# Optimization experiments

Measured on AMD Instinct MI355X. Metric: run time of the kernel, lower is better.

The kernel has to match this reference:

```python
import jax, jax.numpy as jnp
import numpy as np

B, C, H, W = 4, 256, 64, 64
HID = C // 2


def setup_inputs() -> dict:
    key = jax.random.key(0)
    kx, kp, kt, kg, km = jax.random.split(key, 5)
    return {
        "x": jax.random.normal(kx, (B, C, H, W), dtype=jnp.float32),
        "w_phi": jax.random.normal(kp, (HID, C), dtype=jnp.float32) * 0.02,
        "w_theta": jax.random.normal(kt, (HID, C), dtype=jnp.float32) * 0.02,
        "w_g": jax.random.normal(kg, (HID, C), dtype=jnp.float32) * 0.02,
        "w_mask": jax.random.normal(km, (C, HID), dtype=jnp.float32) * 0.02,
    }


def reference(x, w_phi, w_theta, w_g, w_mask):
    b, c, h, w = x.shape
    n = h * w
    xf = x.reshape(b, c, n)                     # [B,C,N]
    # 1x1 convs == channel GEMMs
    phi = jnp.einsum('oc,bcn->bon', w_phi, xf)      # [B,HID,N]
    theta = jnp.einsum('oc,bcn->bon', w_theta, xf)  # [B,HID,N]
    g = jnp.einsum('oc,bcn->bon', w_g, xf)          # [B,HID,N]
    # attn[b,n,m] = sum_c theta[b,c,n] * phi[b,c,m]   (theta^T @ phi)
    attn = jnp.einsum('bcn,bcm->bnm', theta, phi)   # [B,N,N]
    # Faithful to nn.Softmax(dim=1): normalize over axis 1 (theta index)
    attn = jax.nn.softmax(attn, axis=1)
    # attn_g[b,n,c] = sum_m attn[b,n,m] * g[b,c,m]   (attn @ g^T)
    attn_g = jnp.einsum('bnm,bcm->bcn', attn, g)    # [B,HID,N] (already transposed back)
    mask = jnp.einsum('oc,bcn->bon', w_mask, attn_g).reshape(b, c, h, w)
    return mask + x
```

## Files before the change

kernel.cpp:

```cpp
#include <hip/hip_runtime.h>


#define NB   4
#define CIN  256
#define HIDN 128
#define NPIX 4096

typedef __attribute__((ext_vector_type(8))) short short8;
typedef __attribute__((ext_vector_type(4))) float f32x4;
typedef __attribute__((ext_vector_type(16))) float f32x16;

__device__ __forceinline__ unsigned short f2bf(float f) {
    unsigned u = __builtin_bit_cast(unsigned, f);
    u += 0x7fffu + ((u >> 16) & 1u);
    return (unsigned short)(u >> 16);
}
__device__ __forceinline__ unsigned f2bf2(float lo, float hi) {
    return (unsigned)f2bf(lo) | ((unsigned)f2bf(hi) << 16);
}
__device__ __forceinline__ float bf2f(unsigned short s) {
    return __builtin_bit_cast(float, (unsigned)s << 16);
}
__device__ __forceinline__ void cp16(void* lds, const void* g) {
    __builtin_amdgcn_global_load_lds(
        (const __attribute__((address_space(1))) unsigned int*)g,
        (__attribute__((address_space(3))) unsigned int*)lds, 16, 0, 0);
}

__global__ __launch_bounds__(256) void k_prep_w(
    const float* __restrict__ wp, const float* __restrict__ wt,
    const float* __restrict__ wg, const float* __restrict__ wm,
    unsigned short* __restrict__ Wp, unsigned short* __restrict__ Wt,
    unsigned short* __restrict__ Wg, unsigned short* __restrict__ Wm)
{
    const int which = blockIdx.x >> 3;
    const float* src = (which == 0) ? wp : (which == 1) ? wt : (which == 2) ? wg : wm;
    unsigned short* dst = (which == 0) ? Wp : (which == 1) ? Wt : (which == 2) ? Wg : Wm;
#pragma unroll
    for (int t = 0; t < 2; ++t) {
        const int gidx = ((blockIdx.x & 7) * 256 + threadIdx.x) * 2 + t;
        int o, srcc, dstc;
        if (which < 3) {
            o = gidx >> 5;
            const int gc = gidx & 31;
            const int sg = (gc & ~15) | ((gc & 15) ^ (o & 15));
            srcc = o * 256 + gc * 8; dstc = o * 256 + sg * 8;
        } else {
            o = gidx >> 4;
            const int gc = gidx & 15;
            const int sg = gc ^ (o & 15);
            srcc = o * 128 + gc * 8; dstc = o * 128 + sg * 8;
        }
        float4 a = *(const float4*)&src[srcc];
        float4 b = *(const float4*)&src[srcc + 4];
        uint4 v;
        v.x = f2bf2(a.x, a.y); v.y = f2bf2(a.z, a.w);
        v.z = f2bf2(b.x, b.y); v.w = f2bf2(b.z, b.w);
        *(uint4*)&dst[dstc] = v;
    }
}

__global__ __launch_bounds__(256) void k_prep_x(
    const float* __restrict__ x,
    unsigned short* __restrict__ xT,
    float* __restrict__ colsum)
{
    const int nt = blockIdx.x, ct = blockIdx.y, b = blockIdx.z;
    const int tid = threadIdx.x;
    if (ct == 0 && tid < 64) colsum[(size_t)b * NPIX + nt * 64 + tid] = 0.f;

    __shared__ unsigned short Ls[64][66];
    {
        const int c_loc = tid >> 2, n_seg = (tid & 3) * 16;
        const float* src = x + ((size_t)(b * CIN + ct * 64 + c_loc)) * NPIX + nt * 64 + n_seg;
#pragma unroll
        for (int j = 0; j < 8; ++j)
            *(unsigned*)&Ls[c_loc][n_seg + 2 * j] = f2bf2(src[2 * j], src[2 * j + 1]);
    }
    __syncthreads();
    {
        const int n_loc = tid >> 2, c_seg = (tid & 3) * 16;
        const int n_glob = nt * 64 + n_loc;
        unsigned short tmp[16];
#pragma unroll
        for (int j = 0; j < 16; ++j) tmp[j] = Ls[c_seg + j][n_loc];
#pragma unroll
        for (int gr = 0; gr < 2; ++gr) {
            const int c_base = ct * 64 + c_seg + gr * 8;
            const int sec = c_base >> 7;
            const int sg = (((c_base >> 3) & 15) ^ (n_glob & 15));
            *(uint4*)&xT[((size_t)b * NPIX + n_glob) * CIN + sec * 128 + sg * 8] =
                *(uint4*)&tmp[gr * 8];
        }
    }
}

__global__ __launch_bounds__(256, 3) void k_proj(
    const unsigned short* __restrict__ Wp,
    const unsigned short* __restrict__ Wt,
    const unsigned short* __restrict__ Wg,
    const unsigned short* __restrict__ xT,
    unsigned short* __restrict__ phiT,
    unsigned short* __restrict__ thetaT,
    unsigned short* __restrict__ gbuf)
{
    const int nt = blockIdx.x, ot = blockIdx.y, b = blockIdx.z;
    const unsigned short* W = (ot == 0) ? Wp : (ot == 1) ? Wt : Wg;

    __shared__ alignas(16) unsigned short Aw[128][128];
    __shared__ alignas(16) unsigned short Bx[64][128];

    const int tid = threadIdx.x;
    const int wave = tid >> 6, lane = tid & 63;
    const int oh = wave >> 1, nh = wave & 1;
    const int l31 = lane & 31, lh = lane >> 5;
    const int key = l31 & 15;

    f32x16 acc[2];
#pragma unroll
    for (int r = 0; r < 16; ++r) { acc[0][r] = 0.f; acc[1][r] = 0.f; }

    for (int kh = 0; kh < 2; ++kh) {
        __syncthreads();
#pragma unroll
        for (int i = 0; i < 8; ++i) {
            const int u = i * 256 + tid;
            cp16(&Aw[0][0] + u * 8, W + (u >> 4) * 256 + kh * 128 + (u & 15) * 8);
        }
#pragma unroll
        for (int i = 0; i < 4; ++i) {
            const int u = i * 256 + tid;
            cp16(&Bx[0][0] + u * 8,
                 xT + ((size_t)b * NPIX + nt * 64 + (u >> 4)) * CIN + kh * 128 + (u & 15) * 8);
        }
        __syncthreads();
#pragma unroll
        for (int ks = 0; ks < 8; ++ks) {
            const int g = ((ks * 2 + lh) ^ key) << 3;
            short8 bb = *(const short8*)&Bx[nh * 32 + l31][g];
#pragma unroll
            for (int t = 0; t < 2; ++t) {
                short8 a = *(const short8*)&Aw[oh * 64 + t * 32 + l31][g];
                acc[t] = __builtin_amdgcn_mfma_f32_32x32x16_bf16(a, bb, acc[t], 0, 0, 0);
            }
        }
    }

    const int n_glob = nt * 64 + nh * 32 + l31;
    if (ot < 2) {
        unsigned short* T = (ot == 0) ? phiT : thetaT;
#pragma unroll
        for (int t = 0; t < 2; ++t)
#pragma unroll
            for (int rg = 0; rg < 4; ++rg) {
                const int ob = oh * 64 + t * 32 + 8 * rg + 4 * lh;
                const int sc = (((ob >> 3) ^ (n_glob & 15)) << 3) | (ob & 7);
                uint2 v;
                v.x = f2bf2(acc[t][rg * 4 + 0], acc[t][rg * 4 + 1]);
                v.y = f2bf2(acc[t][rg * 4 + 2], acc[t][rg * 4 + 3]);
                *(uint2*)&T[((size_t)b * NPIX + n_glob) * HIDN + sc] = v;
            }
    } else {
        const int sbase = n_glob & ~63;
        const int g8 = (n_glob >> 3) & 7, c7off = n_glob & 7;
#pragma unroll
        for (int t = 0; t < 2; ++t)
#pragma unroll
            for (int r = 0; r < 16; ++r) {
                const int c = oh * 64 + t * 32 + (r & 3) + 8 * (r >> 2) + 4 * lh;
                const int sc = sbase | (((g8 ^ (c & 7)) << 3)) | c7off;
                gbuf[((size_t)b * HIDN + c) * NPIX + sc] = f2bf(acc[t][r]);
            }
    }
}

__global__ __launch_bounds__(256, 3) void k_colsum(
    const unsigned short* __restrict__ thetaT,
    const unsigned short* __restrict__ phiT,
    float* __restrict__ colsum,
    float* __restrict__ O32)
{
    const int mt = blockIdx.x, ng = blockIdx.y, b = blockIdx.z;
    const int tid = threadIdx.x;
    {
        const int blin = ((blockIdx.z * 8 + blockIdx.y) * 32 + blockIdx.x);
        float* p = O32 + (size_t)blin * 2048 + tid * 8;
        *(f32x4*)p = f32x4{0.f, 0.f, 0.f, 0.f};
        *(f32x4*)(p + 4) = f32x4{0.f, 0.f, 0.f, 0.f};
    }

    __shared__ alignas(16) unsigned short As[64][128];

    const int wave = tid >> 6, lane = tid & 63;
    const int wn = wave & 1, wh = wave >> 1;
    const int l31 = lane & 31, lh = lane >> 5;
    const int key = l31 & 15;

    short8 bfrag[2][8];
#pragma unroll
    for (int t = 0; t < 2; ++t) {
        const int m = mt * 128 + wn * 64 + t * 32 + l31;
        const unsigned short* src = phiT + ((size_t)b * NPIX + m) * HIDN;
#pragma unroll
        for (int ks = 0; ks < 8; ++ks)
            bfrag[t][ks] = *(const short8*)(src + (((ks * 2 + lh) ^ key) << 3));
    }

    float csum[2] = {0.f, 0.f};

    for (int nc = 0; nc < 8; ++nc) {
        const int n0 = ng * 512 + nc * 64;
        __syncthreads();
#pragma unroll
        for (int i = 0; i < 4; ++i) {
            const int u = i * 256 + tid;
            cp16(&As[0][0] + u * 8,
                 thetaT + ((size_t)b * NPIX + n0 + (u >> 4)) * HIDN + (u & 15) * 8);
        }
        __syncthreads();

        f32x16 acc[2];
#pragma unroll
        for (int r = 0; r < 16; ++r) { acc[0][r] = 0.f; acc[1][r] = 0.f; }
#pragma unroll
        for (int ks = 0; ks < 8; ++ks) {
            short8 a = *(const short8*)&As[wh * 32 + l31][(((ks * 2 + lh) ^ key) << 3)];
            acc[0] = __builtin_amdgcn_mfma_f32_32x32x16_bf16(a, bfrag[0][ks], acc[0], 0, 0, 0);
            acc[1] = __builtin_amdgcn_mfma_f32_32x32x16_bf16(a, bfrag[1][ks], acc[1], 0, 0, 0);
        }
#pragma unroll
        for (int t = 0; t < 2; ++t)
#pragma unroll
            for (int r = 0; r < 16; ++r) csum[t] += __expf(acc[t][r]);
    }

#pragma unroll
    for (int t = 0; t < 2; ++t) {
        float s = csum[t];
        s += __shfl_xor(s, 32);
        if (lh == 0)
            atomicAdd(&colsum[(size_t)b * NPIX + mt * 128 + wn * 64 + t * 32 + l31], s);
    }
}

__global__ __launch_bounds__(256) void k_scale_g(
    unsigned short* __restrict__ gbuf, const float* __restrict__ colsum)
{
    const int idx = blockIdx.x * 256 + threadIdx.x;
    const int row = idx >> 9;
    const int sc = (idx & 511) * 8;
    const int bb = row >> 7;
    const int mt = (sc & ~63) | (((((sc >> 3) & 7) ^ (row & 7))) << 3);
    uint4 v = *(uint4*)&gbuf[(size_t)row * NPIX + sc];
    float4 c0 = *(const float4*)&colsum[(size_t)bb * NPIX + mt];
    float4 c1 = *(const float4*)&colsum[(size_t)bb * NPIX + mt + 4];
    unsigned short* vs = (unsigned short*)&v;
    const float cs[8] = {c0.x, c0.y, c0.z, c0.w, c1.x, c1.y, c1.z, c1.w};
#pragma unroll
    for (int j = 0; j < 8; ++j) vs[j] = f2bf(bf2f(vs[j]) / cs[j]);
    *(uint4*)&gbuf[(size_t)row * NPIX + sc] = v;
}

__global__ __launch_bounds__(256, 4) void k_attn(
    const unsigned short* __restrict__ thetaT,
    const unsigned short* __restrict__ phiT,
    const unsigned short* __restrict__ gbuf,
    float* __restrict__ O32)
{
    const int nt = blockIdx.x, ms = blockIdx.y, b = blockIdx.z;
    const int n0 = nt * 64;

    __shared__ alignas(16) unsigned short Bs[64][128];
    __shared__ alignas(16) unsigned short Gs[128][64];
    __shared__ alignas(16) unsigned short Ps[64][64];

    const int tid = threadIdx.x;
    const int wave = tid >> 6, lane = tid & 63;
    const int wm = wave >> 1, wn = wave & 1;
    const int l31 = lane & 31, lh = lane >> 5;
    const int key = l31 & 15, key7 = l31 & 7;

    short8 afrag[8];
    {
        const unsigned short* src = thetaT + ((size_t)b * NPIX + n0 + wm * 32 + l31) * HIDN;
#pragma unroll
        for (int ks = 0; ks < 8; ++ks)
            afrag[ks] = *(const short8*)(src + (((ks * 2 + lh) ^ key) << 3));
    }

    f32x16 accO[2];
#pragma unroll
    for (int r = 0; r < 16; ++r) { accO[0][r] = 0.f; accO[1][r] = 0.f; }

    for (int mc = 0; mc < 16; ++mc) {
        const int m0 = (ms * 16 + mc) * 64;
        __syncthreads();
#pragma unroll
        for (int i = 0; i < 4; ++i) {
            const int u = i * 256 + tid;
            cp16(&Bs[0][0] + u * 8,
                 phiT + ((size_t)b * NPIX + m0 + (u >> 4)) * HIDN + (u & 15) * 8);
        }
#pragma unroll
        for (int i = 0; i < 4; ++i) {
            const int u = i * 256 + tid;
            cp16(&Gs[0][0] + u * 8,
                 gbuf + ((size_t)b * HIDN + (u >> 3)) * NPIX + m0 + (u & 7) * 8);
        }
        __syncthreads();

        f32x16 accS;
#pragma unroll
        for (int r = 0; r < 16; ++r) accS[r] = 0.f;
#pragma unroll
        for (int ks = 0; ks < 8; ++ks) {
            short8 bb = *(const short8*)&Bs[wn * 32 + l31][(((ks * 2 + lh) ^ key) << 3)];
            accS = __builtin_amdgcn_mfma_f32_32x32x16_bf16(afrag[ks], bb, accS, 0, 0, 0);
        }
        {
            const int m_loc = wn * 32 + l31;
#pragma unroll
            for (int r = 0; r < 16; ++r) {
                const int n_loc = wm * 32 + (r & 3) + 8 * (r >> 2) + 4 * lh;
                const int sc = (((m_loc >> 3) ^ (n_loc & 7)) << 3) | (m_loc & 7);
                Ps[n_loc][sc] = f2bf(__expf(accS[r]));
            }
        }
        __syncthreads();
#pragma unroll
        for (int ks = 0; ks < 4; ++ks) {
            const int g = ((ks * 2 + lh) ^ key7) << 3;
            short8 pa = *(const short8*)&Ps[wm * 32 + l31][g];
            short8 g0 = *(const short8*)&Gs[wn * 64 + l31][g];
            short8 g1 = *(const short8*)&Gs[wn * 64 + 32 + l31][g];
            accO[0] = __builtin_amdgcn_mfma_f32_32x32x16_bf16(pa, g0, accO[0], 0, 0, 0);
            accO[1] = __builtin_amdgcn_mfma_f32_32x32x16_bf16(pa, g1, accO[1], 0, 0, 0);
        }
    }

#pragma unroll
    for (int t = 0; t < 2; ++t)
#pragma unroll
        for (int r = 0; r < 16; ++r) {
            const int n = n0 + wm * 32 + (r & 3) + 8 * (r >> 2) + 4 * lh;
            const int c = wn * 64 + t * 32 + l31;
            atomicAdd(&O32[((size_t)b * NPIX + n) * HIDN + c], accO[t][r]);
        }
}

__global__ __launch_bounds__(256, 3) void k_mask(
    const unsigned short* __restrict__ Wm,
    const float* __restrict__ O32,
    const float* __restrict__ x,
    float* __restrict__ out)
{
    const int nt = blockIdx.x, ct = blockIdx.y, b = blockIdx.z;
    __shared__ alignas(16) unsigned short As[128][128];
    __shared__ alignas(16) unsigned short Bs[64][128];

    const int tid = threadIdx.x;
    const int wave = tid >> 6, lane = tid & 63;
    const int oh = wave >> 1, nh = wave & 1;
    const int l31 = lane & 31, lh = lane >> 5;
    const int key = l31 & 15;

#pragma unroll
    for (int i = 0; i < 8; ++i) {
        const int u = i * 256 + tid;
        cp16(&As[0][0] + u * 8, Wm + (ct * 128 + (u >> 4)) * HIDN + (u & 15) * 8);
    }
    {
        const int n_loc = tid >> 2, seg = (tid & 3) * 32;
        const float* src = O32 + ((size_t)b * NPIX + nt * 64 + n_loc) * HIDN + seg;
        const int k7 = n_loc & 7;
#pragma unroll
        for (int j = 0; j < 4; ++j) {
            const int gr = (seg >> 3) + j;
            const int sg = (gr & ~7) | ((gr & 7) ^ k7);
            const float* s8 = src + j * 8;
            unsigned* d = (unsigned*)&Bs[n_loc][sg * 8];
#pragma unroll
            for (int k = 0; k < 4; ++k) d[k] = f2bf2(s8[2 * k], s8[2 * k + 1]);
        }
    }
    __syncthreads();

    f32x16 acc[2];
#pragma unroll
    for (int r = 0; r < 16; ++r) { acc[0][r] = 0.f; acc[1][r] = 0.f; }
#pragma unroll
    for (int ks = 0; ks < 8; ++ks) {
        const int gr = ks * 2 + lh;
        const int sgb = ((gr & ~7) | ((gr & 7) ^ (l31 & 7))) << 3;
        short8 bb = *(const short8*)&Bs[nh * 32 + l31][sgb];
#pragma unroll
        for (int t = 0; t < 2; ++t) {
            short8 a = *(const short8*)&As[oh * 64 + t * 32 + l31][((gr ^ key) << 3)];
            acc[t] = __builtin_amdgcn_mfma_f32_32x32x16_bf16(a, bb, acc[t], 0, 0, 0);
        }
    }

    const int n = nt * 64 + nh * 32 + l31;
#pragma unroll
    for (int t = 0; t < 2; ++t)
#pragma unroll
        for (int r = 0; r < 16; ++r) {
            const int co = ct * 128 + oh * 64 + t * 32 + (r & 3) + 8 * (r >> 2) + 4 * lh;
            const size_t idx = ((size_t)b * CIN + co) * NPIX + n;
            out[idx] = acc[t][r] + x[idx];
        }
}

extern "C" void kernel_launch(void* const* d_in, const int* in_sizes, int n_in,
                              void* d_out, int out_size, void* d_ws, size_t ws_size,
                              hipStream_t stream)
{
    (void)in_sizes; (void)n_in; (void)out_size; (void)ws_size;
    const float* x       = (const float*)d_in[0];
    const float* w_phi   = (const float*)d_in[1];
    const float* w_theta = (const float*)d_in[2];
    const float* w_g     = (const float*)d_in[3];
    const float* w_mask  = (const float*)d_in[4];
    float* out = (float*)d_out;

    char* ws = (char*)d_ws;
    unsigned short* phiT   = (unsigned short*)(ws);
    unsigned short* thetaT = (unsigned short*)(ws + 4194304);
    unsigned short* gbuf   = (unsigned short*)(ws + 8388608);
    float*          colsum = (float*)(ws + 12582912);
    unsigned short* xT     = (unsigned short*)(ws + 12648448);
    float*          O32    = (float*)(ws + 12648448);
    unsigned short* Wp     = (unsigned short*)(ws + 21037056);
    unsigned short* Wt     = (unsigned short*)(ws + 21102592);
    unsigned short* Wg     = (unsigned short*)(ws + 21168128);
    unsigned short* Wm     = (unsigned short*)(ws + 21233664);

    k_prep_w <<<dim3(32),        256, 0, stream>>>(w_phi, w_theta, w_g, w_mask, Wp, Wt, Wg, Wm);
    k_prep_x <<<dim3(64, 4, 4),  256, 0, stream>>>(x, xT, colsum);
    k_proj   <<<dim3(64, 3, 4),  256, 0, stream>>>(Wp, Wt, Wg, xT, phiT, thetaT, gbuf);
    k_colsum <<<dim3(32, 8, 4),  256, 0, stream>>>(thetaT, phiT, colsum, O32);
    k_scale_g<<<dim3(1024),      256, 0, stream>>>(gbuf, colsum);
    k_attn   <<<dim3(64, 4, 4),  256, 0, stream>>>(thetaT, phiT, gbuf, O32);
    k_mask   <<<dim3(64, 2, 4),  256, 0, stream>>>(Wm, O32, x, out);
}
```

Baseline: 186.5 us.

## Restructure attention kernel: theta tile in LDS, phi in registers, 128-wide m chunks

The attention kernel now keeps the 64-row theta tile resident in shared memory and streams phi directly into registers, prefetching the next chunk's phi fragments while the current chunk is processed. Each iteration covers 128 key positions instead of 64, with a larger G tile and a padded P tile. The g buffer swizzle widens from 8 to 16 groups to match the new tile width. The grid's m-split halves, giving fewer blocks, fewer O32 atomics and fewer barriers per unit of work, at the cost of more LDS and registers and lower occupancy (launch bound 2).

```diff
diff --git a/kernel.cpp b/kernel.cpp
--- a/kernel.cpp
+++ b/kernel.cpp
@@ -161,14 +161,14 @@
                 *(uint2*)&T[((size_t)b * NPIX + n_glob) * HIDN + sc] = v;
             }
     } else {
-        const int sbase = n_glob & ~63;
-        const int g8 = (n_glob >> 3) & 7, c7off = n_glob & 7;
+        const int sbase = n_glob & ~127;
+        const int g16 = (n_glob >> 3) & 15, c7off = n_glob & 7;
 #pragma unroll
         for (int t = 0; t < 2; ++t)
 #pragma unroll
             for (int r = 0; r < 16; ++r) {
                 const int c = oh * 64 + t * 32 + (r & 3) + 8 * (r >> 2) + 4 * lh;
-                const int sc = sbase | (((g8 ^ (c & 7)) << 3)) | c7off;
+                const int sc = sbase | ((g16 ^ (c & 15)) << 3) | c7off;
                 gbuf[((size_t)b * HIDN + c) * NPIX + sc] = f2bf(acc[t][r]);
             }
     }
@@ -250,7 +250,7 @@
     const int row = idx >> 9;
     const int sc = (idx & 511) * 8;
     const int bb = row >> 7;
-    const int mt = (sc & ~63) | (((((sc >> 3) & 7) ^ (row & 7))) << 3);
+    const int mt = (sc & ~127) | ((((sc >> 3) & 15) ^ (row & 15)) << 3);
     uint4 v = *(uint4*)&gbuf[(size_t)row * NPIX + sc];
     float4 c0 = *(const float4*)&colsum[(size_t)bb * NPIX + mt];
     float4 c1 = *(const float4*)&colsum[(size_t)bb * NPIX + mt + 4];
@@ -261,7 +261,7 @@
     *(uint4*)&gbuf[(size_t)row * NPIX + sc] = v;
 }
 
-__global__ __launch_bounds__(256, 4) void k_attn(
+__global__ __launch_bounds__(256, 2) void k_attn(
     const unsigned short* __restrict__ thetaT,
     const unsigned short* __restrict__ phiT,
     const unsigned short* __restrict__ gbuf,
@@ -270,80 +270,101 @@
     const int nt = blockIdx.x, ms = blockIdx.y, b = blockIdx.z;
     const int n0 = nt * 64;
 
-    __shared__ alignas(16) unsigned short Bs[64][128];
-    __shared__ alignas(16) unsigned short Gs[128][64];
-    __shared__ alignas(16) unsigned short Ps[64][64];
+    __shared__ alignas(16) unsigned short Ts[64][128];
+    __shared__ alignas(16) unsigned short Gs[128][128];
+    __shared__ alignas(16) unsigned short Ps[64][136];
 
     const int tid = threadIdx.x;
     const int wave = tid >> 6, lane = tid & 63;
-    const int wm = wave >> 1, wn = wave & 1;
+    const int q = wave;
+    const int nh = wave >> 1, ch = wave & 1;
     const int l31 = lane & 31, lh = lane >> 5;
-    const int key = l31 & 15, key7 = l31 & 7;
-
-    short8 afrag[8];
+    const int key = l31 & 15;
+
+#pragma unroll
+    for (int i = 0; i < 4; ++i) {
+        const int u = i * 256 + tid;
+        cp16(&Ts[0][0] + u * 8,
+             thetaT + ((size_t)b * NPIX + n0 + (u >> 4)) * HIDN + (u & 15) * 8);
+    }
+
+    short8 pcur[8], pnxt[8];
     {
-        const unsigned short* src = thetaT + ((size_t)b * NPIX + n0 + wm * 32 + l31) * HIDN;
+        const unsigned short* src = phiT + ((size_t)b * NPIX + ms * 2048 + q * 32 + l31) * HIDN;
 #pragma unroll
         for (int ks = 0; ks < 8; ++ks)
-            afrag[ks] = *(const short8*)(src + (((ks * 2 + lh) ^ key) << 3));
+            pcur[ks] = *(const short8*)(src + (((ks * 2 + lh) ^ key) << 3));
     }
 
     f32x16 accO[2];
 #pragma unroll
     for (int r = 0; r < 16; ++r) { accO[0][r] = 0.f; accO[1][r] = 0.f; }
 
+    __syncthreads();
+
     for (int mc = 0; mc < 16; ++mc) {
-        const int m0 = (ms * 16 + mc) * 64;
-        __syncthreads();
-#pragma unroll
-        for (int i = 0; i < 4; ++i) {
-            const int u = i * 256 + tid;
-            cp16(&Bs[0][0] + u * 8,
-                 phiT + ((size_t)b * NPIX + m0 + (u >> 4)) * HIDN + (u & 15) * 8);
-        }
-#pragma unroll
-        for (int i = 0; i < 4; ++i) {
+        const int m0 = ms * 2048 + mc * 128;
+#pragma unroll
+        for (int i = 0; i < 8; ++i) {
             const int u = i * 256 + tid;
             cp16(&Gs[0][0] + u * 8,
-                 gbuf + ((size_t)b * HIDN + (u >> 3)) * NPIX + m0 + (u & 7) * 8);
-        }
-        __syncthreads();
-
-        f32x16 accS;
-#pragma unroll
-        for (int r = 0; r < 16; ++r) accS[r] = 0.f;
+                 gbuf + ((size_t)b * HIDN + (u >> 4)) * NPIX + m0 + (u & 15) * 8);
+        }
+        if (mc < 15) {
+            const unsigned short* src =
+                phiT + ((size_t)b * NPIX + m0 + 128 + q * 32 + l31) * HIDN;
+#pragma unroll
+            for (int ks = 0; ks < 8; ++ks)
+                pnxt[ks] = *(const short8*)(src + (((ks * 2 + lh) ^ key) << 3));
+        }
+
+        f32x16 accS[2];
+#pragma unroll
+        for (int r = 0; r < 16; ++r) { accS[0][r] = 0.f; accS[1][r] = 0.f; }
 #pragma unroll
         for (int ks = 0; ks < 8; ++ks) {
-            short8 bb = *(const short8*)&Bs[wn * 32 + l31][(((ks * 2 + lh) ^ key) << 3)];
-            accS = __builtin_amdgcn_mfma_f32_32x32x16_bf16(afrag[ks], bb, accS, 0, 0, 0);
-        }
-        {
-            const int m_loc = wn * 32 + l31;
-#pragma unroll
-            for (int r = 0; r < 16; ++r) {
-                const int n_loc = wm * 32 + (r & 3) + 8 * (r >> 2) + 4 * lh;
-                const int sc = (((m_loc >> 3) ^ (n_loc & 7)) << 3) | (m_loc & 7);
-                Ps[n_loc][sc] = f2bf(__expf(accS[r]));
+            const int g = ((ks * 2 + lh) ^ key) << 3;
+            short8 t0 = *(const short8*)&Ts[l31][g];
+            short8 t1 = *(const short8*)&Ts[32 + l31][g];
+            accS[0] = __builtin_amdgcn_mfma_f32_32x32x16_bf16(pcur[ks], t0, accS[0], 0, 0, 0);
+            accS[1] = __builtin_amdgcn_mfma_f32_32x32x16_bf16(pcur[ks], t1, accS[1], 0, 0, 0);
+        }
+#pragma unroll
+        for (int t = 0; t < 2; ++t) {
+            const int n = t * 32 + l31;
+#pragma unroll
+            for (int rg = 0; rg < 4; ++rg) {
+                uint2 v;
+                v.x = f2bf2(__expf(accS[t][rg * 4 + 0]), __expf(accS[t][rg * 4 + 1]));
+                v.y = f2bf2(__expf(accS[t][rg * 4 + 2]), __expf(accS[t][rg * 4 + 3]));
+                const int gm = q * 4 + rg;
+                const int col = (((gm ^ (n & 15)) << 3) | (4 * lh));
+                *(uint2*)&Ps[n][col] = v;
             }
         }
         __syncthreads();
-#pragma unroll
-        for (int ks = 0; ks < 4; ++ks) {
-            const int g = ((ks * 2 + lh) ^ key7) << 3;
-            short8 pa = *(const short8*)&Ps[wm * 32 + l31][g];
-            short8 g0 = *(const short8*)&Gs[wn * 64 + l31][g];
-            short8 g1 = *(const short8*)&Gs[wn * 64 + 32 + l31][g];
+
+#pragma unroll
+        for (int ks = 0; ks < 8; ++ks) {
+            const int g = ((ks * 2 + lh) ^ key) << 3;
+            short8 pa = *(const short8*)&Ps[nh * 32 + l31][g];
+            short8 g0 = *(const short8*)&Gs[ch * 64 + l31][g];
+            short8 g1 = *(const short8*)&Gs[ch * 64 + 32 + l31][g];
             accO[0] = __builtin_amdgcn_mfma_f32_32x32x16_bf16(pa, g0, accO[0], 0, 0, 0);
             accO[1] = __builtin_amdgcn_mfma_f32_32x32x16_bf16(pa, g1, accO[1], 0, 0, 0);
         }
+        __syncthreads();
+
+#pragma unroll
+        for (int ks = 0; ks < 8; ++ks) pcur[ks] = pnxt[ks];
     }
 
 #pragma unroll
     for (int t = 0; t < 2; ++t)
 #pragma unroll
         for (int r = 0; r < 16; ++r) {
-            const int n = n0 + wm * 32 + (r & 3) + 8 * (r >> 2) + 4 * lh;
-            const int c = wn * 64 + t * 32 + l31;
+            const int n = n0 + nh * 32 + (r & 3) + 8 * (r >> 2) + 4 * lh;
+            const int c = ch * 64 + t * 32 + l31;
             atomicAdd(&O32[((size_t)b * NPIX + n) * HIDN + c], accO[t][r]);
         }
 }
@@ -440,6 +461,6 @@
     k_proj   <<<dim3(64, 3, 4),  256, 0, stream>>>(Wp, Wt, Wg, xT, phiT, thetaT, gbuf);
     k_colsum <<<dim3(32, 8, 4),  256, 0, stream>>>(thetaT, phiT, colsum, O32);
     k_scale_g<<<dim3(1024),      256, 0, stream>>>(gbuf, colsum);
-    k_attn   <<<dim3(64, 4, 4),  256, 0, stream>>>(thetaT, phiT, gbuf, O32);
+    k_attn   <<<dim3(64, 2, 4),  256, 0, stream>>>(thetaT, phiT, gbuf, O32);
     k_mask   <<<dim3(64, 2, 4),  256, 0, stream>>>(Wm, O32, x, out);
 }
```

Result: slower. 193.9 us (+4.0%).
